# Kernel tuning notes

Hardware: AMD Instinct MI355X
Metric: run time of the kernel (lower is better)

## Reference

```python
import jax, jax.numpy as jnp
import numpy as np

H, KVH, D, EPS = 8, 4, 64, 1e-5

def _rmsnorm(x, w):
    # normalize over last dim (head_dim)
    norm = jax.lax.rsqrt(jnp.mean(x * x, axis=-1, keepdims=True) + EPS)
    return x * norm * w

def setup_inputs() -> dict:
    key = jax.random.key(0)
    ks = jax.random.split(key, 5)
    B, S, Hid = 2048, 67, 512
    x = jax.random.normal(ks[0], (B, S, Hid), dtype=jnp.float32)
    # weights stored as [in, out] (equivalent to torch Linear weight.T)
    sc = 1.0 / np.sqrt(Hid)
    wq = jax.random.normal(ks[1], (Hid, H * D), dtype=jnp.float32) * sc
    wk = jax.random.normal(ks[2], (Hid, KVH * D), dtype=jnp.float32) * sc
    wv = jax.random.normal(ks[3], (Hid, KVH * D), dtype=jnp.float32) * sc
    wo = jax.random.normal(ks[4], (H * D, Hid), dtype=jnp.float32) * sc
    q_norm_w = jnp.ones((D,), dtype=jnp.float32)
    k_norm_w = jnp.ones((D,), dtype=jnp.float32)
    return {"x": x, "wq": wq, "wk": wk, "wv": wv, "wo": wo,
            "q_norm_w": q_norm_w, "k_norm_w": k_norm_w}

def reference(x, wq, wk, wv, wo, q_norm_w, k_norm_w):
    B, S, _ = x.shape
    G = H // KVH  # query heads per kv head
    q = (x @ wq).reshape(B, S, H, D).transpose(0, 2, 1, 3)      # (B,H,S,D)
    k = (x @ wk).reshape(B, S, KVH, D).transpose(0, 2, 1, 3)    # (B,KVH,S,D)
    v = (x @ wv).reshape(B, S, KVH, D).transpose(0, 2, 1, 3)
    q = _rmsnorm(q, q_norm_w)
    k = _rmsnorm(k, k_norm_w)
    qg = q.reshape(B, KVH, G, S, D)
    scale = 1.0 / np.sqrt(D)
    # bidirectional GQA attention, no mask
    scores = jnp.einsum('bkgsd,bktd->bkgst', qg, k) * scale      # (B,KVH,G,S,S)
    attn = jax.nn.softmax(scores, axis=-1)
    out = jnp.einsum('bkgst,bktd->bkgsd', attn, v)               # (B,KVH,G,S,D)
    out = out.reshape(B, H, S, D).transpose(0, 2, 1, 3).reshape(B, S, H * D)
    return out @ wo
```

## Files before the change

kernel.cpp:

```cpp
#include <hip/hip_runtime.h>
#include <hip/hip_bf16.h>

typedef __attribute__((ext_vector_type(8))) short short8;
typedef __attribute__((ext_vector_type(4))) float f32x4;

#define B_   2048
#define S_   67
#define M_   (B_*S_)
#define HID_ 512
#define H_   8
#define KVH_ 4
#define D_   64

__device__ __forceinline__ unsigned f2bf_u(float f){
  union { __hip_bfloat16 h; unsigned short u; } c; c.h = __float2bfloat16(f); return (unsigned)c.u;
}
__device__ __forceinline__ float bfu2f(unsigned u){
  union { unsigned short u; __hip_bfloat16 h; } c; c.u = (unsigned short)u; return __bfloat162float(c.h);
}
__device__ __forceinline__ unsigned pack2(float a, float b){ return f2bf_u(a) | (f2bf_u(b) << 16); }

__device__ __forceinline__ void unpack8(uint4 v, float* o){
  o[0]=bfu2f(v.x & 0xffffu); o[1]=bfu2f(v.x >> 16);
  o[2]=bfu2f(v.y & 0xffffu); o[3]=bfu2f(v.y >> 16);
  o[4]=bfu2f(v.z & 0xffffu); o[5]=bfu2f(v.z >> 16);
  o[6]=bfu2f(v.w & 0xffffu); o[7]=bfu2f(v.w >> 16);
}

union S8 { short8 v; unsigned short u[8]; };

__global__ __launch_bounds__(256) void cvt_bf16(const float* __restrict__ src,
                                                unsigned short* __restrict__ dst){
  long i = (long)blockIdx.x*256 + threadIdx.x;
  const float4 a = reinterpret_cast<const float4*>(src)[2*i];
  const float4 b = reinterpret_cast<const float4*>(src)[2*i+1];
  uint4 u = { pack2(a.x,a.y), pack2(a.z,a.w), pack2(b.x,b.y), pack2(b.z,b.w) };
  reinterpret_cast<uint4*>(dst)[i] = u;
}

__global__ __launch_bounds__(256) void transpose_w(const float* __restrict__ src, int ncols,
                                                   unsigned short* __restrict__ dst, int row0){
  __shared__ float tile[32][33];
  const int tx = threadIdx.x & 31, ty = threadIdx.x >> 5;
  const int nb = blockIdx.x * 32, kb = blockIdx.y * 32;
  #pragma unroll
  for (int i = 0; i < 4; ++i){
    int r = ty + i*8;
    tile[r][tx] = src[(size_t)(kb + r)*ncols + nb + tx];
  }
  __syncthreads();
  #pragma unroll
  for (int i = 0; i < 4; ++i){
    int r = ty + i*8;
    dst[(size_t)(row0 + nb + r)*512 + kb + tx] = (unsigned short)f2bf_u(tile[tx][r]);
  }
}

template<bool OUT_F32>
__global__ __launch_bounds__(256, 4) void gemm4_k(const unsigned short* __restrict__ A,
                                                  const unsigned short* __restrict__ Bw,
                                                  void* __restrict__ outp, int nbx){
  __shared__ unsigned short Sh[2][2][128*32];

  const int Nld = nbx << 7;
  const int per = gridDim.x >> 3;
  const int wg  = (blockIdx.x & 7) * per + (blockIdx.x >> 3);
  const int m0 = (wg / nbx) * 128;
  const int n0 = (wg % nbx) * 128;

  const int t = threadIdx.x;
  const int l = t & 63;
  const int w = t >> 6;
  const int wr = w >> 1, wc = w & 1;
  const int lr = l & 15, lk = l >> 4;

  const int srow = w*32 + (l >> 2);
  const int sblk = (l & 3) ^ (srow & 3) ^ ((srow >> 2) & 3);
  const unsigned short* Ag = A  + (size_t)(m0 + srow)*512 + sblk*8;
  const unsigned short* Bg = Bw + (size_t)(n0 + srow)*512 + sblk*8;

  f32x4 acc[4][4];
  #pragma unroll
  for (int f = 0; f < 4; ++f)
    #pragma unroll
    for (int g = 0; g < 4; ++g) acc[f][g] = (f32x4){0.f, 0.f, 0.f, 0.f};

#define STAGE_(tt) do{ \
    unsigned short* As_ = &Sh[(tt)&1][0][0]; \
    unsigned short* Bs_ = &Sh[(tt)&1][1][0]; \
    _Pragma("unroll") \
    for (int j = 0; j < 2; ++j){ \
      __builtin_amdgcn_global_load_lds((const unsigned int*)(Ag + (size_t)(j*16)*512 + (tt)*32), \
                                       (unsigned int*)(As_ + (w*32 + j*16)*32), 16, 0, 0); \
      __builtin_amdgcn_global_load_lds((const unsigned int*)(Bg + (size_t)(j*16)*512 + (tt)*32), \
                                       (unsigned int*)(Bs_ + (w*32 + j*16)*32), 16, 0, 0); \
    } }while(0)

  STAGE_(0);
  #pragma unroll
  for (int tt = 0; tt < 16; ++tt){
    if (tt < 15) STAGE_(tt + 1);
    if (tt < 15) asm volatile("s_waitcnt vmcnt(4)" ::: "memory");
    else         asm volatile("s_waitcnt vmcnt(0)" ::: "memory");
    __builtin_amdgcn_s_barrier();
    __builtin_amdgcn_sched_barrier(0);

    const unsigned short* As = &Sh[tt&1][0][0];
    const unsigned short* Bs = &Sh[tt&1][1][0];
    const int pk = (lk ^ (lr & 3) ^ ((lr >> 2) & 3)) * 8;
    short8 av[4], bv[4];
    #pragma unroll
    for (int f = 0; f < 4; ++f){
      av[f] = *reinterpret_cast<const short8*>(As + (wr*64 + f*16 + lr)*32 + pk);
      bv[f] = *reinterpret_cast<const short8*>(Bs + (wc*64 + f*16 + lr)*32 + pk);
    }
    __builtin_amdgcn_s_setprio(1);
    #pragma unroll
    for (int f = 0; f < 4; ++f)
      #pragma unroll
      for (int g = 0; g < 4; ++g)
        acc[f][g] = __builtin_amdgcn_mfma_f32_16x16x32_bf16(av[f], bv[g], acc[f][g], 0, 0, 0);
    __builtin_amdgcn_s_setprio(0);
    asm volatile("s_waitcnt lgkmcnt(0)" ::: "memory");
    __builtin_amdgcn_sched_barrier(0);
    __builtin_amdgcn_s_barrier();
  }
#undef STAGE_

  if (OUT_F32){
    float* out = (float*)outp;
    #pragma unroll
    for (int f = 0; f < 4; ++f)
      #pragma unroll
      for (int g = 0; g < 4; ++g)
        #pragma unroll
        for (int r = 0; r < 4; ++r){
          size_t row = (size_t)(m0 + wr*64 + f*16 + lk*4 + r);
          out[row*Nld + n0 + wc*64 + g*16 + lr] = acc[f][g][r];
        }
  } else {
    __syncthreads();
    unsigned short* Cs = &Sh[0][0][0];
    #pragma unroll
    for (int f = 0; f < 4; ++f)
      #pragma unroll
      for (int g = 0; g < 4; ++g)
        #pragma unroll
        for (int r = 0; r < 4; ++r){
          int row = wr*64 + f*16 + lk*4 + r;
          int col = wc*64 + g*16 + lr;
          Cs[row*128 + col] = (unsigned short)f2bf_u(acc[f][g][r]);
        }
    __syncthreads();
    unsigned short* out = (unsigned short*)outp;
    const uint4* Cv = reinterpret_cast<const uint4*>(Cs);
    #pragma unroll
    for (int p = 0; p < 8; ++p){
      int idx = p*256 + t;
      int row = idx >> 4, c8 = idx & 15;
      *reinterpret_cast<uint4*>(out + (size_t)(m0 + row)*Nld + n0 + c8*8) = Cv[idx];
    }
  }
}

__global__ __launch_bounds__(576, 5) void attn_k(const unsigned short* __restrict__ qkv,
                                                 const float* __restrict__ qnw,
                                                 const float* __restrict__ knw,
                                                 unsigned short* __restrict__ attn){
  __shared__ unsigned short Vt[64*128];
  __shared__ unsigned short Kf[5][2][64*8];
  __shared__ unsigned short Pb[9][16*128];
  const int t = threadIdx.x;
  const int b = blockIdx.x >> 2, kvh = blockIdx.x & 3;
  const size_t rowbase = (size_t)b * 67;
  const int l = t & 63, w = t >> 6;
  const int lr = l & 15, lk = l >> 4;

  const int vs = t >> 3, vd0 = (t & 7) << 3;
  uint4 vu = {0u,0u,0u,0u};
  if (vs < 67)
    vu = *reinterpret_cast<const uint4*>(qkv + (rowbase + vs)*1024 + 768 + kvh*64 + vd0);
  uint4 ku0 = {0u,0u,0u,0u}, ku1 = {0u,0u,0u,0u};
  if (w < 5){
    int s = w*16 + lr; if (s > 66) s = 66;
    const unsigned short* kp = qkv + (rowbase + s)*1024 + 512 + kvh*64 + lk*8;
    ku0 = *reinterpret_cast<const uint4*>(kp);
    ku1 = *reinterpret_cast<const uint4*>(kp + 32);
  }
  const int qrow = w*16 + lr;
  const int h01 = (qrow >= 67) ? 1 : 0;
  int qr = qrow - (h01 ? 67 : 0); if (qr > 66) qr = 66;
  const unsigned short* qp = qkv + (rowbase + qr)*1024 + (kvh*2 + h01)*64 + lk*8;
  const uint4 qu0 = *reinterpret_cast<const uint4*>(qp);
  const uint4 qu1 = *reinterpret_cast<const uint4*>(qp + 32);
  float wp[16];
  #pragma unroll
  for (int hh = 0; hh < 2; ++hh)
    #pragma unroll
    for (int j = 0; j < 8; ++j){
      int idx = hh*32 + lk*8 + j;
      wp[hh*8+j] = qnw[idx] * knw[idx] * 0.125f;
    }

  {
    unsigned short vsv[8];
    vsv[0]=vu.x&0xffffu; vsv[1]=vu.x>>16; vsv[2]=vu.y&0xffffu; vsv[3]=vu.y>>16;
    vsv[4]=vu.z&0xffffu; vsv[5]=vu.z>>16; vsv[6]=vu.w&0xffffu; vsv[7]=vu.w>>16;
    #pragma unroll
    for (int j = 0; j < 8; ++j){
      int d = vd0 + j;
      int blk = ((vs>>3) ^ (j<<1) ^ (t&7)) & 15;
      Vt[(d<<7) + (blk<<3) + (vs&7)] = vsv[j];
    }
    if (t < 192){
      int s2 = 72 + (t >> 3);
      #pragma unroll
      for (int j = 0; j < 8; ++j){
        int d = vd0 + j;
        int blk = ((s2>>3) ^ (j<<1) ^ (t&7)) & 15;
        Vt[(d<<7) + (blk<<3) + (s2&7)] = 0;
      }
    }
  }

  if (w < 5){
    float f[16]; unpack8(ku0, f); unpack8(ku1, f + 8);
    float ss = 0.f;
    #pragma unroll
    for (int j = 0; j < 16; ++j) ss += f[j]*f[j];
    ss += __shfl_xor(ss, 16); ss += __shfl_xor(ss, 32);
    float inv = rsqrtf(ss*(1.0f/64.0f) + 1e-5f);
    S8 a0, a1;
    #pragma unroll
    for (int j = 0; j < 8; ++j){
      a0.u[j] = (unsigned short)f2bf_u(f[j]   * inv * wp[j]);
      a1.u[j] = (unsigned short)f2bf_u(f[8+j] * inv * wp[8+j]);
    }
    *reinterpret_cast<short8*>(&Kf[w][0][l*8]) = a0.v;
    *reinterpret_cast<short8*>(&Kf[w][1][l*8]) = a1.v;
  }

  short8 qf0, qf1;
  {
    float f[16]; unpack8(qu0, f); unpack8(qu1, f + 8);
    float ss = 0.f;
    #pragma unroll
    for (int j = 0; j < 16; ++j) ss += f[j]*f[j];
    ss += __shfl_xor(ss, 16); ss += __shfl_xor(ss, 32);
    float inv = rsqrtf(ss*(1.0f/64.0f) + 1e-5f);
    S8 a0, a1;
    #pragma unroll
    for (int j = 0; j < 8; ++j){
      a0.u[j] = (unsigned short)f2bf_u(f[j]   * inv);
      a1.u[j] = (unsigned short)f2bf_u(f[8+j] * inv);
    }
    qf0 = a0.v; qf1 = a1.v;
  }

  {
    uint4 z = {0u,0u,0u,0u};
    uint4* pz = reinterpret_cast<uint4*>(Pb[w]);
    #pragma unroll
    for (int i = 0; i < 4; ++i) pz[l + i*64] = z;
  }
  __syncthreads();

  f32x4 sa[5];
  #pragma unroll
  for (int nt = 0; nt < 5; ++nt){
    short8 k0 = *reinterpret_cast<const short8*>(&Kf[nt][0][l*8]);
    short8 k1 = *reinterpret_cast<const short8*>(&Kf[nt][1][l*8]);
    sa[nt] = (f32x4){0.f,0.f,0.f,0.f};
    sa[nt] = __builtin_amdgcn_mfma_f32_16x16x32_bf16(qf0, k0, sa[nt], 0,0,0);
    sa[nt] = __builtin_amdgcn_mfma_f32_16x16x32_bf16(qf1, k1, sa[nt], 0,0,0);
  }

  float inv4[4];
  #pragma unroll
  for (int r = 0; r < 4; ++r){
    float mx = -1e30f;
    #pragma unroll
    for (int nt = 0; nt < 5; ++nt){
      float v = sa[nt][r];
      if (nt*16 + lr >= 67) v = -1e30f;
      sa[nt][r] = v; mx = fmaxf(mx, v);
    }
    mx = fmaxf(mx, __shfl_xor(mx, 1));
    mx = fmaxf(mx, __shfl_xor(mx, 2));
    mx = fmaxf(mx, __shfl_xor(mx, 4));
    mx = fmaxf(mx, __shfl_xor(mx, 8));
    float sm = 0.f;
    #pragma unroll
    for (int nt = 0; nt < 5; ++nt){
      float e = __expf(sa[nt][r] - mx);
      sa[nt][r] = e; sm += e;
    }
    sm += __shfl_xor(sm, 1);
    sm += __shfl_xor(sm, 2);
    sm += __shfl_xor(sm, 4);
    sm += __shfl_xor(sm, 8);
    inv4[r] = 1.0f / sm;
  }

  unsigned short* pb = Pb[w];
  #pragma unroll
  for (int nt = 0; nt < 5; ++nt)
    #pragma unroll
    for (int r = 0; r < 4; ++r){
      int row = lk*4 + r, col = nt*16 + lr;
      int blk = ((col>>3) ^ ((row&7)<<1) ^ (row>>3)) & 15;
      pb[(row<<7) + (blk<<3) + (col&7)] = (unsigned short)f2bf_u(sa[nt][r]);
    }

  f32x4 oa[4];
  #pragma unroll
  for (int dt = 0; dt < 4; ++dt) oa[dt] = (f32x4){0.f,0.f,0.f,0.f};
  #pragma unroll
  for (int ks = 0; ks < 3; ++ks){
    int blkp = ((ks*4 + lk) ^ ((lr&7)<<1) ^ (lr>>3)) & 15;
    short8 pf = *reinterpret_cast<const short8*>(&pb[(lr<<7) + (blkp<<3)]);
    #pragma unroll
    for (int dt = 0; dt < 4; ++dt){
      int d = dt*16 + lr;
      int blkv = ((ks*4 + lk) ^ ((d&7)<<1) ^ (d>>3)) & 15;
      short8 vf = *reinterpret_cast<const short8*>(&Vt[(d<<7) + (blkv<<3)]);
      oa[dt] = __builtin_amdgcn_mfma_f32_16x16x32_bf16(pf, vf, oa[dt], 0,0,0);
    }
  }

  #pragma unroll
  for (int dt = 0; dt < 4; ++dt)
    #pragma unroll
    for (int r = 0; r < 4; ++r){
      int row = w*16 + lk*4 + r;
      if (row < 134){
        int hh = (row >= 67) ? 1 : 0;
        int orow = row - (hh ? 67 : 0);
        attn[(rowbase + orow)*512 + (kvh*2 + hh)*64 + dt*16 + lr] =
            (unsigned short)f2bf_u(oa[dt][r] * inv4[r]);
      }
    }
}

extern "C" void kernel_launch(void* const* d_in, const int* in_sizes, int n_in,
                              void* d_out, int out_size, void* d_ws, size_t ws_size,
                              hipStream_t stream){
  const float* x   = (const float*)d_in[0];
  const float* wq  = (const float*)d_in[1];
  const float* wk  = (const float*)d_in[2];
  const float* wv  = (const float*)d_in[3];
  const float* wo  = (const float*)d_in[4];
  const float* qnw = (const float*)d_in[5];
  const float* knw = (const float*)d_in[6];

  unsigned short* Wt   = (unsigned short*)d_ws;
  unsigned short* Wot  = Wt + 1024*512;
  unsigned short* qkv  = Wot + 512*512;
  unsigned short* attn = qkv + (size_t)M_*1024;
  unsigned short* xb   = attn;

  transpose_w<<<dim3(16,16), 256, 0, stream>>>(wq, 512, Wt, 0);
  transpose_w<<<dim3(8,16),  256, 0, stream>>>(wk, 256, Wt, 512);
  transpose_w<<<dim3(8,16),  256, 0, stream>>>(wv, 256, Wt, 768);
  transpose_w<<<dim3(16,16), 256, 0, stream>>>(wo, 512, Wot, 0);

  cvt_bf16<<<(M_*512/8)/256, 256, 0, stream>>>(x, xb);

  gemm4_k<false><<<dim3(8 * (M_/128)), 256, 0, stream>>>(xb, Wt, qkv, 8);

  attn_k<<<dim3(B_*KVH_), 576, 0, stream>>>(qkv, qnw, knw, attn);

  gemm4_k<true><<<dim3(4 * (M_/128)), 256, 0, stream>>>(attn, Wot, d_out, 4);
}
```

Before: 586.8 us.

## Fuse fp32-to-bf16 input conversion into the QKV projection GEMM

Drops the separate cvt_bf16 pass over x. A new GEMM kernel loads fp32 A tiles straight into LDS with a swizzled layout and converts them to bf16 in registers before the MFMA. This avoids writing and re-reading a bf16 copy of the whole activation tensor. In exchange, each GEMM block reads twice as many A bytes from global memory, uses a larger LDS footprint with fewer blocks per CU (launch bounds 3), and adds conversion ALU work in the inner loop.

Measured after the change: 604.6 us. 3.0% more time.

```diff
diff --git a/kernel.cpp b/kernel.cpp
--- a/kernel.cpp
+++ b/kernel.cpp
@@ -29,15 +29,6 @@
 
 union S8 { short8 v; unsigned short u[8]; };
 
-__global__ __launch_bounds__(256) void cvt_bf16(const float* __restrict__ src,
-                                                unsigned short* __restrict__ dst){
-  long i = (long)blockIdx.x*256 + threadIdx.x;
-  const float4 a = reinterpret_cast<const float4*>(src)[2*i];
-  const float4 b = reinterpret_cast<const float4*>(src)[2*i+1];
-  uint4 u = { pack2(a.x,a.y), pack2(a.z,a.w), pack2(b.x,b.y), pack2(b.z,b.w) };
-  reinterpret_cast<uint4*>(dst)[i] = u;
-}
-
 __global__ __launch_bounds__(256) void transpose_w(const float* __restrict__ src, int ncols,
                                                    unsigned short* __restrict__ dst, int row0){
   __shared__ float tile[32][33];
@@ -53,6 +44,113 @@
   for (int i = 0; i < 4; ++i){
     int r = ty + i*8;
     dst[(size_t)(row0 + nb + r)*512 + kb + tx] = (unsigned short)f2bf_u(tile[tx][r]);
+  }
+}
+
+__global__ __launch_bounds__(256, 3) void gemm6_k(const float* __restrict__ A,
+                                                  const unsigned short* __restrict__ Bw,
+                                                  unsigned short* __restrict__ outp, int nbx){
+  __shared__ unsigned short ShA[2][128*64];
+  __shared__ unsigned short ShB[2][128*32];
+
+  const int Nld = nbx << 7;
+  const int per = gridDim.x >> 3;
+  const int wg  = (blockIdx.x & 7) * per + (blockIdx.x >> 3);
+  const int m0 = (wg / nbx) * 128;
+  const int n0 = (wg % nbx) * 128;
+
+  const int t = threadIdx.x;
+  const int l = t & 63;
+  const int w = t >> 6;
+  const int wr = w >> 1, wc = w & 1;
+  const int lr = l & 15, lk = l >> 4;
+
+  const int arow = w*32 + (l >> 3);
+  const int afoff = (((((l & 7) >> 1) ^ (arow & 3)) << 3) + (l & 1)*4);
+  const float* Ag = A + (size_t)(m0 + arow)*512 + afoff;
+  const int brow = w*32 + (l >> 2);
+  const int bblk = (l & 3) ^ (brow & 3) ^ ((brow >> 2) & 3);
+  const unsigned short* Bg = Bw + (size_t)(n0 + brow)*512 + bblk*8;
+
+  f32x4 acc[4][4];
+  #pragma unroll
+  for (int f = 0; f < 4; ++f)
+    #pragma unroll
+    for (int g = 0; g < 4; ++g) acc[f][g] = (f32x4){0.f, 0.f, 0.f, 0.f};
+
+#define STAGE6_(tt) do{ \
+    unsigned short* As_ = &ShA[(tt)&1][0]; \
+    unsigned short* Bs_ = &ShB[(tt)&1][0]; \
+    _Pragma("unroll") \
+    for (int j = 0; j < 4; ++j) \
+      __builtin_amdgcn_global_load_lds((const unsigned int*)(Ag + (size_t)(j*8)*512 + (tt)*32), \
+                                       (unsigned int*)(As_ + (w*32 + j*8)*64), 16, 0, 0); \
+    _Pragma("unroll") \
+    for (int j = 0; j < 2; ++j) \
+      __builtin_amdgcn_global_load_lds((const unsigned int*)(Bg + (size_t)(j*16)*512 + (tt)*32), \
+                                       (unsigned int*)(Bs_ + (w*32 + j*16)*32), 16, 0, 0); \
+  }while(0)
+
+  STAGE6_(0);
+  #pragma unroll
+  for (int tt = 0; tt < 16; ++tt){
+    if (tt < 15) STAGE6_(tt + 1);
+    if (tt < 15) asm volatile("s_waitcnt vmcnt(6)" ::: "memory");
+    else         asm volatile("s_waitcnt vmcnt(0)" ::: "memory");
+    __builtin_amdgcn_s_barrier();
+    __builtin_amdgcn_sched_barrier(0);
+
+    const unsigned short* As = &ShA[tt&1][0];
+    const unsigned short* Bs = &ShB[tt&1][0];
+    const int pkb = (lk ^ (lr & 3) ^ ((lr >> 2) & 3)) * 8;
+    const int pka = (lk ^ (lr & 3)) * 16;
+    short8 av[4], bv[4];
+    #pragma unroll
+    for (int f = 0; f < 4; ++f){
+      const float* ap = reinterpret_cast<const float*>(As + (wr*64 + f*16 + lr)*64 + pka);
+      f32x4 lo = *reinterpret_cast<const f32x4*>(ap);
+      f32x4 hi = *reinterpret_cast<const f32x4*>(ap + 4);
+      S8 a;
+      #pragma unroll
+      for (int j = 0; j < 4; ++j){
+        a.u[j]   = (unsigned short)f2bf_u(lo[j]);
+        a.u[4+j] = (unsigned short)f2bf_u(hi[j]);
+      }
+      av[f] = a.v;
+      bv[f] = *reinterpret_cast<const short8*>(Bs + (wc*64 + f*16 + lr)*32 + pkb);
+    }
+    __builtin_amdgcn_s_setprio(1);
+    #pragma unroll
+    for (int f = 0; f < 4; ++f)
+      #pragma unroll
+      for (int g = 0; g < 4; ++g)
+        acc[f][g] = __builtin_amdgcn_mfma_f32_16x16x32_bf16(av[f], bv[g], acc[f][g], 0, 0, 0);
+    __builtin_amdgcn_s_setprio(0);
+    asm volatile("s_waitcnt lgkmcnt(0)" ::: "memory");
+    __builtin_amdgcn_sched_barrier(0);
+    __builtin_amdgcn_s_barrier();
+  }
+#undef STAGE6_
+
+  __syncthreads();
+  unsigned short* Cs = &ShA[0][0];
+  #pragma unroll
+  for (int f = 0; f < 4; ++f)
+    #pragma unroll
+    for (int g = 0; g < 4; ++g)
+      #pragma unroll
+      for (int r = 0; r < 4; ++r){
+        int row = wr*64 + f*16 + lk*4 + r;
+        int col = wc*64 + g*16 + lr;
+        Cs[row*128 + col] = (unsigned short)f2bf_u(acc[f][g][r]);
+      }
+  __syncthreads();
+  const uint4* Cv = reinterpret_cast<const uint4*>(Cs);
+  #pragma unroll
+  for (int p = 0; p < 8; ++p){
+    int idx = p*256 + t;
+    int row = idx >> 4, c8 = idx & 15;
+    *reinterpret_cast<uint4*>(outp + (size_t)(m0 + row)*Nld + n0 + c8*8) = Cv[idx];
   }
 }
 
@@ -357,16 +455,13 @@
   unsigned short* Wot  = Wt + 1024*512;
   unsigned short* qkv  = Wot + 512*512;
   unsigned short* attn = qkv + (size_t)M_*1024;
-  unsigned short* xb   = attn;
 
   transpose_w<<<dim3(16,16), 256, 0, stream>>>(wq, 512, Wt, 0);
   transpose_w<<<dim3(8,16),  256, 0, stream>>>(wk, 256, Wt, 512);
   transpose_w<<<dim3(8,16),  256, 0, stream>>>(wv, 256, Wt, 768);
   transpose_w<<<dim3(16,16), 256, 0, stream>>>(wo, 512, Wot, 0);
 
-  cvt_bf16<<<(M_*512/8)/256, 256, 0, stream>>>(x, xb);
-
-  gemm4_k<false><<<dim3(8 * (M_/128)), 256, 0, stream>>>(xb, Wt, qkv, 8);
+  gemm6_k<<<dim3(8 * (M_/128)), 256, 0, stream>>>(x, Wt, qkv, 8);
 
   attn_k<<<dim3(B_*KVH_), 576, 0, stream>>>(qkv, qnw, knw, attn);
 
```
